# Performance work log

Measured on AMD Instinct MI355X. Metric: run time of the kernel, lower is better.

## Reference

```python
import jax, jax.numpy as jnp
import numpy as np

B, T, N, M = 64, 128, 128, 512


def setup_inputs() -> dict:
    key = jax.random.key(0)
    ks = jax.random.split(key, 9)
    w = 0.02
    return dict(
        X=jax.random.normal(ks[0], (B, T, N), jnp.float32),
        h0=jax.random.normal(ks[1], (B, M), jnp.float32) * 0.05,
        s0=jax.random.normal(ks[2], (B, M), jnp.float32) * 0.05,
        # LSTM cell params (keras gate order: i, f, c, o)
        W_lstm=jax.random.normal(ks[3], (N, 4 * M), jnp.float32) * w,
        U_lstm=jax.random.normal(ks[4], (M, 4 * M), jnp.float32) * w,
        b_lstm=jnp.zeros((4 * M,), jnp.float32),
        # InputAttention params: W_e: Dense(T) on concat([h,c]) (2m -> T),
        # U_e: Dense(T) on X^T (T -> T), v_e: Dense(1) (T -> 1)
        W_e=jax.random.normal(ks[5], (2 * M, T), jnp.float32) * w,
        b_We=jnp.zeros((T,), jnp.float32),
        U_e=jax.random.normal(ks[6], (T, T), jnp.float32) * w,
        b_Ue=jnp.zeros((T,), jnp.float32),
        v_e=jax.random.normal(ks[7], (T, 1), jnp.float32) * w,
        b_ve=jnp.zeros((1,), jnp.float32),
    )


def reference(X, h0, s0, W_lstm, U_lstm, b_lstm, W_e, b_We, U_e, b_Ue, v_e, b_ve):
    # In the original, every loop iteration t runs a single LSTM step on
    # X[:, t, :] starting from the SAME initial_state [h0, s0] (state is not
    # carried across t), so all T steps are independent -> vectorize over T.
    z = jnp.einsum('btn,nk->btk', X, W_lstm) + (h0 @ U_lstm + b_lstm)[:, None, :]
    zi, zf, zc, zo = jnp.split(z, 4, axis=-1)  # keras gate order i,f,c,o
    i = jax.nn.sigmoid(zi)
    f = jax.nn.sigmoid(zf)
    o = jax.nn.sigmoid(zo)
    c = f * s0[:, None, :] + i * jnp.tanh(zc)  # (B, T, m)
    h = o * jnp.tanh(c)                        # (B, T, m)

    # InputAttention for every t at once:
    # e_t = v_e(tanh(W_e([h_t; c_t]) broadcast over n  +  U_e(X^T)))
    hc = jnp.concatenate([h, c], axis=-1)              # (B, T, 2m)
    A = hc @ W_e + b_We                                # (B, T, T)
    U = jnp.einsum('btn,tk->bnk', X, U_e) + b_Ue       # (B, n, T)
    e = jnp.tanh(A[:, :, None, :] + U[:, None, :, :])  # (B, T, n, T)
    scores = jnp.einsum('btnk,k->btn', e, v_e[:, 0]) + b_ve[0]  # (B, T, n)
    alpha = jax.nn.softmax(scores, axis=-1)            # softmax over n
    return X * alpha
```

## Files before the change

kernel.cpp:

```cpp
#include <hip/hip_runtime.h>

typedef __attribute__((ext_vector_type(8))) short bfrag;
typedef __attribute__((ext_vector_type(4))) float f32x4;

#define C_SCALE 2.885390081777926815f

__device__ __forceinline__ float fast_rcp(float x){
#if __has_builtin(__builtin_amdgcn_rcpf)
  return __builtin_amdgcn_rcpf(x);
#else
  return 1.0f/x;
#endif
}
__device__ __forceinline__ float fexp2(float x){
#if __has_builtin(__builtin_amdgcn_exp2f)
  return __builtin_amdgcn_exp2f(x);
#else
  return exp2f(x);
#endif
}
__device__ __forceinline__ float sigm(float x){ return fast_rcp(1.0f + __expf(-x)); }
__device__ __forceinline__ float tanh_f(float x){ return 1.0f - 2.0f*fast_rcp(__expf(2.0f*x) + 1.0f); }
__device__ __forceinline__ unsigned short f2bf(float f){
  unsigned u = __float_as_uint(f);
  return (unsigned short)((u + 0x7fffu + ((u>>16)&1u)) >> 16);
}
__device__ __forceinline__ void gload16(const void* g, void* l){
  __builtin_amdgcn_global_load_lds((const __attribute__((address_space(1))) void*)g,
                                   (__attribute__((address_space(3))) void*)l, 16, 0, 0);
}

__global__ __launch_bounds__(256) void prep(const float* __restrict__ X,
                                            unsigned short* __restrict__ Xbf,
                                            const float* __restrict__ Wl,
                                            unsigned short* __restrict__ Wlt,
                                            const float* __restrict__ We,
                                            unsigned short* __restrict__ Wet,
                                            const float* __restrict__ h0,
                                            const float* __restrict__ Ul,
                                            float* __restrict__ Uhp,
                                            const float* __restrict__ Ue,
                                            const float* __restrict__ bUe,
                                            unsigned short* __restrict__ UTb){
  __shared__ __align__(16) float sh[6600];
  const int tid = threadIdx.x;
  const int bid = blockIdx.x;

  if (bid < 512){
    const int i = (bid*256 + tid)*8;
    float4 a = *(const float4*)&X[i];
    float4 b = *(const float4*)&X[i+4];
    ushort4 lo, hi;
    lo.x=f2bf(a.x); lo.y=f2bf(a.y); lo.z=f2bf(a.z); lo.w=f2bf(a.w);
    hi.x=f2bf(b.x); hi.y=f2bf(b.y); hi.z=f2bf(b.z); hi.w=f2bf(b.w);
    *(ushort4*)&Xbf[i] = lo; *(ushort4*)&Xbf[i+4] = hi;
  } else if (bid < 608){
    const float* in; unsigned short* outp; int K, N, j0, k0, perm;
    if (bid < 576){ int r = bid-512; in = Wl; outp = Wlt; K = 128;  N = 2048; j0 = (r&31)*64; k0 = (r>>5)*64; perm = 0; }
    else          { int r = bid-576; in = We; outp = Wet; K = 1024; N = 128;  j0 = (r&1)*64;  k0 = (r>>1)*64; perm = 1; }
    float (*t)[68] = (float(*)[68])sh;
#pragma unroll
    for (int i=0;i<4;i++){
      int idx = tid + i*256;
      int r = idx>>4, c4 = idx&15;
      int kk = k0 + r;
      int srow = perm ? ((kk&1) ? 512 + (kk>>1) : (kk>>1)) : kk;
      *(float4*)&t[r][c4*4] = *(const float4*)&in[srow*N + j0 + c4*4];
    }
    __syncthreads();
#pragma unroll
    for (int i=0;i<4;i++){
      int idx = tid + i*256;
      int r = idx>>4, c4 = idx&15;
      ushort4 o;
      o.x = f2bf(t[c4*4+0][r]); o.y = f2bf(t[c4*4+1][r]);
      o.z = f2bf(t[c4*4+2][r]); o.w = f2bf(t[c4*4+3][r]);
      *(ushort4*)&outp[(j0+r)*K + k0 + c4*4] = o;
    }
  } else if (bid < 736){
    const int r = bid - 608;
    const int nh = r & 1, b = r >> 1;
    float (*Xs)[68]  = (float(*)[68])sh;
    float (*Us)[132] = (float(*)[132])(sh + 2176);
    const int tc5 = tid & 31, tr8 = tid >> 5;
    f32x4 a4[8];
#pragma unroll
    for (int j=0;j<8;j++) a4[j] = (f32x4){0.f,0.f,0.f,0.f};
    for (int tk=0; tk<4; tk++){
#pragma unroll
      for (int i=0;i<2;i++){
        int idx = tid + i*256;
        int t = idx>>4, nq = idx&15;
        *(float4*)&Xs[t][nq*4] = *(const float4*)&X[(b*128 + tk*32 + t)*128 + nh*64 + nq*4];
      }
#pragma unroll
      for (int i=0;i<4;i++){
        int idx = tid + i*256;
        int t = idx>>5, kq = idx&31;
        *(float4*)&Us[t][kq*4] = *(const float4*)&Ue[(tk*32+t)*128 + kq*4];
      }
      __syncthreads();
#pragma unroll 4
      for (int t=0;t<32;t++){
        f32x4 u4 = *(const f32x4*)&Us[t][tc5*4];
        f32x4 x0 = *(const f32x4*)&Xs[t][tr8*8];
        f32x4 x1 = *(const f32x4*)&Xs[t][tr8*8+4];
        a4[0] += x0.x*u4; a4[1] += x0.y*u4; a4[2] += x0.z*u4; a4[3] += x0.w*u4;
        a4[4] += x1.x*u4; a4[5] += x1.y*u4; a4[6] += x1.z*u4; a4[7] += x1.w*u4;
      }
      __syncthreads();
    }
    const f32x4 bu = *(const f32x4*)&bUe[tc5*4];
    const int ktile = tc5 >> 1, khalf = tc5 & 1;
#pragma unroll
    for (int j=0;j<8;j++){
      const int n = nh*64 + tr8*8 + j;
      f32x4 v = a4[j] + bu;
      ushort4 o;
      o.x = f2bf(fexp2(C_SCALE*v.x)); o.y = f2bf(fexp2(C_SCALE*v.y));
      o.z = f2bf(fexp2(C_SCALE*v.z)); o.w = f2bf(fexp2(C_SCALE*v.w));
      *(ushort4*)&UTb[b*16384 + ktile*1024 + n*8 + khalf*4] = o;
    }
  } else {
    const int r = bid - 736;
    const int jc = r & 15;
    const int bc = (r>>4) >> 2, kc = (r>>4) & 3;
    float (*h0s)[128] = (float(*)[128])sh;
#pragma unroll
    for (int i=0;i<2;i++){
      int idx = tid + i*256;
      int bi = idx>>5, kq = idx&31;
      *(float4*)&h0s[bi][kq*4] = *(const float4*)&h0[(bc*16+bi)*512 + kc*128 + kq*4];
    }
    __syncthreads();
    const int jj = tid & 127, bh = tid >> 7;
    const int j = jc*128 + jj;
    float acc[8];
#pragma unroll
    for (int i=0;i<8;i++) acc[i]=0.f;
    for (int k=0;k<128;k+=4){
      float w0 = Ul[(kc*128+k+0)*2048 + j];
      float w1 = Ul[(kc*128+k+1)*2048 + j];
      float w2 = Ul[(kc*128+k+2)*2048 + j];
      float w3 = Ul[(kc*128+k+3)*2048 + j];
#pragma unroll
      for (int bi=0;bi<8;bi++){
        float4 h4 = *(const float4*)&h0s[bh*8+bi][k];
        acc[bi] += h4.x*w0 + h4.y*w1 + h4.z*w2 + h4.w*w3;
      }
    }
#pragma unroll
    for (int bi=0;bi<8;bi++)
      Uhp[kc*131072 + (bc*16 + bh*8 + bi)*2048 + j] = acc[bi];
  }
}

__global__ __launch_bounds__(256) void k2_k(const unsigned short* __restrict__ Xbf,
                                            const unsigned short* __restrict__ Wlt,
                                            const float* __restrict__ Uhp,
                                            const float* __restrict__ bl,
                                            const float* __restrict__ s0,
                                            unsigned int* __restrict__ hci){
  __shared__ __align__(16) char lds[32768];
  const int tid = threadIdx.x;
  const int mc = blockIdx.x & 15, b = blockIdx.x >> 4;
  const int bt0 = b*128;
  const int lane = tid & 63, wave = tid >> 6;
  const int wr = wave >> 1, wc = wave & 1;

  f32x4 acc[4][4];
#pragma unroll
  for (int mt=0;mt<4;mt++)
#pragma unroll
    for (int nt=0;nt<4;nt++) acc[mt][nt] = (f32x4){0.f,0.f,0.f,0.f};

  for (int kh=0; kh<2; kh++){
#pragma unroll
    for (int i=0;i<4;i++){
      int g = tid + i*256;
      int r = g>>3, G = g&7;
      gload16(Xbf + (bt0+r)*128 + kh*64 + ((G ^ (r&7))<<3), lds + g*16);
    }
#pragma unroll
    for (int i=0;i<4;i++){
      int g = tid + i*256;
      int c = g>>3, G = g&7;
      int q = c>>4;
      int j = (q&3)*512 + mc*32 + ((q>>2)<<4) + (c&15);
      gload16(Wlt + j*128 + kh*64 + ((G ^ (c&7))<<3), lds + 16384 + g*16);
    }
    __syncthreads();
#pragma unroll
    for (int ks2=0; ks2<2; ks2++){
      const int kb = ks2*64 + ((lane>>4)<<4);
      bfrag a[4], bb[4];
#pragma unroll
      for (int mt=0;mt<4;mt++){
        int r = wr*64 + mt*16 + (lane&15);
        a[mt] = *(const bfrag*)&lds[r*128 + (kb ^ ((r&7)<<4))];
      }
#pragma unroll
      for (int nt=0;nt<4;nt++){
        int c = wc*64 + nt*16 + (lane&15);
        bb[nt] = *(const bfrag*)&lds[16384 + c*128 + (kb ^ ((c&7)<<4))];
      }
#pragma unroll
      for (int mt=0;mt<4;mt++)
#pragma unroll
        for (int nt=0;nt<4;nt++)
          acc[mt][nt] = __builtin_amdgcn_mfma_f32_16x16x32_bf16(a[mt], bb[nt], acc[mt][nt], 0, 0, 0);
    }
    __syncthreads();
  }

  const int mloc = mc*32 + wc*16 + (lane&15);
  float uh[4];
#pragma unroll
  for (int g=0;g<4;g++){
    int j = g*512 + mloc;
    uh[g] = bl[j] + Uhp[0*131072 + b*2048 + j] + Uhp[1*131072 + b*2048 + j]
                  + Uhp[2*131072 + b*2048 + j] + Uhp[3*131072 + b*2048 + j];
  }
  const float s0v = s0[b*512 + mloc];
#pragma unroll
  for (int mt=0;mt<4;mt++){
#pragma unroll
    for (int reg=0;reg<4;reg++){
      int row = wr*64 + mt*16 + (lane>>4)*4 + reg;
      float zi = acc[mt][0][reg] + uh[0];
      float zf = acc[mt][1][reg] + uh[1];
      float zc = acc[mt][2][reg] + uh[2];
      float zo = acc[mt][3][reg] + uh[3];
      float fi = sigm(zi), ff = sigm(zf), fo = sigm(zo);
      float cv = ff*s0v + fi*tanh_f(zc);
      float hv = fo*tanh_f(cv);
      hci[(bt0+row)*512 + mloc] = (unsigned)f2bf(hv) | ((unsigned)f2bf(cv) << 16);
    }
  }
}

__global__ __launch_bounds__(256) void k35(const unsigned short* __restrict__ hc,
                                           const unsigned short* __restrict__ Wet,
                                           const float* __restrict__ bWe,
                                           const float* __restrict__ X,
                                           const unsigned short* __restrict__ UTb,
                                           const float* __restrict__ ve,
                                           float* __restrict__ out){
  __shared__ __align__(16) char ldsA[4096];
  __shared__ __align__(16) char ldsB[32768];
  __shared__ __align__(16) float eAs[16][132];
  __shared__ __align__(16) float vs[128];
  __shared__ float redm[4][8], reds[4][8];
  const int tid = threadIdx.x;
  const int tpc = blockIdx.x;
  const int b   = blockIdx.y;
  const int t0  = tpc*16;
  const int lane = tid & 63, wave = tid >> 6;

  if (tid < 128) vs[tid] = ve[tid];

  f32x4 acc[2];
  acc[0] = (f32x4){0.f,0.f,0.f,0.f};
  acc[1] = (f32x4){0.f,0.f,0.f,0.f};

  for (int ks=0; ks<8; ks++){
    const int k0 = ks*128;
    {
      int r = tid>>4, G = tid&15;
      gload16(hc + (b*128 + t0 + r)*1024 + k0 + ((G ^ (r&7))<<3), ldsA + tid*16);
    }
#pragma unroll
    for (int i=0;i<8;i++){
      int g = tid + i*256;
      int n = g>>4, G = g&15;
      gload16(Wet + n*1024 + k0 + ((G ^ (n&7))<<3), ldsB + g*16);
    }
    __syncthreads();
#pragma unroll
    for (int kk=0;kk<4;kk++){
      const int kb = kk*64 + ((lane>>4)<<4);
      const int r = lane & 15;
      bfrag a = *(const bfrag*)&ldsA[r*256 + (kb ^ ((r&7)<<4))];
      const int c0 = wave*32 + (lane&15);
      bfrag b0 = *(const bfrag*)&ldsB[c0*256 + (kb ^ ((c0&7)<<4))];
      const int c1 = c0 + 16;
      bfrag b1 = *(const bfrag*)&ldsB[c1*256 + (kb ^ ((c1&7)<<4))];
      acc[0] = __builtin_amdgcn_mfma_f32_16x16x32_bf16(a, b0, acc[0], 0, 0, 0);
      acc[1] = __builtin_amdgcn_mfma_f32_16x16x32_bf16(a, b1, acc[1], 0, 0, 0);
    }
    __syncthreads();
  }
#pragma unroll
  for (int nt=0;nt<2;nt++){
    const int col = wave*32 + nt*16 + (lane&15);
    const float bw = bWe[col];
#pragma unroll
    for (int reg=0;reg<4;reg++){
      const int row = (lane>>4)*4 + reg;
      eAs[row][col] = fexp2(C_SCALE*(acc[nt][reg] + bw));
    }
  }
  __syncthreads();

  const int tpair = tid>>7, n = tid&127, wid = tid>>6;
  f32x4 sc[8];
#pragma unroll
  for (int tt=0;tt<8;tt++) sc[tt] = (f32x4){0.f,0.f,0.f,0.f};

  const unsigned short* urow = UTb + b*16384 + n*8;
#pragma unroll 2
  for (int k8=0; k8<16; k8++){
    uint4 u = *(const uint4*)(urow + k8*1024);
    f32x4 ua, ub;
    ua.x = __uint_as_float(u.x<<16); ua.y = __uint_as_float(u.x & 0xffff0000u);
    ua.z = __uint_as_float(u.y<<16); ua.w = __uint_as_float(u.y & 0xffff0000u);
    ub.x = __uint_as_float(u.z<<16); ub.y = __uint_as_float(u.z & 0xffff0000u);
    ub.z = __uint_as_float(u.w<<16); ub.w = __uint_as_float(u.w & 0xffff0000u);
    const f32x4 va = *(const f32x4*)&vs[k8*8];
    const f32x4 vb = *(const f32x4*)&vs[k8*8+4];
#pragma unroll
    for (int tt=0; tt<8; tt++){
      const float* Ar = &eAs[tt*2+tpair][k8*8];
      f32x4 ea = *(const f32x4*)Ar;
      f32x4 eb = *(const f32x4*)(Ar+4);
      f32x4 ra, rb;
      ra.x = fast_rcp(ea.x*ua.x + 1.f); ra.y = fast_rcp(ea.y*ua.y + 1.f);
      ra.z = fast_rcp(ea.z*ua.z + 1.f); ra.w = fast_rcp(ea.w*ua.w + 1.f);
      rb.x = fast_rcp(eb.x*ub.x + 1.f); rb.y = fast_rcp(eb.y*ub.y + 1.f);
      rb.z = fast_rcp(eb.z*ub.z + 1.f); rb.w = fast_rcp(eb.w*ub.w + 1.f);
      sc[tt] += va*ra;
      sc[tt] += vb*rb;
    }
  }

  float sv[8];
#pragma unroll
  for (int tt=0;tt<8;tt++){
    float s = -2.f*((sc[tt].x + sc[tt].y) + (sc[tt].z + sc[tt].w));
    sv[tt] = s;
    float m = s;
#pragma unroll
    for (int off=32; off>0; off>>=1) m = fmaxf(m, __shfl_xor(m, off));
    if ((tid&63)==0) redm[wid][tt] = m;
  }
  __syncthreads();
  float evv[8];
#pragma unroll
  for (int tt=0;tt<8;tt++){
    const float M = fmaxf(redm[tpair*2][tt], redm[tpair*2+1][tt]);
    float e = __expf(sv[tt] - M);
    evv[tt] = e;
    float s = e;
#pragma unroll
    for (int off=32; off>0; off>>=1) s += __shfl_xor(s, off);
    if ((tid&63)==0) reds[wid][tt] = s;
  }
  __syncthreads();
#pragma unroll
  for (int tt=0;tt<8;tt++){
    const float S = reds[tpair*2][tt] + reds[tpair*2+1][tt];
    const float alpha = evv[tt] * fast_rcp(S);
    const int t = t0 + tt*2 + tpair;
    const int g = (b*128 + t)*128 + n;
    out[g] = X[g] * alpha;
  }
}

extern "C" void kernel_launch(void* const* d_in, const int* in_sizes, int n_in,
                              void* d_out, int out_size, void* d_ws, size_t ws_size,
                              hipStream_t stream){
  (void)in_sizes; (void)n_in; (void)out_size; (void)ws_size;
  const float* X   = (const float*)d_in[0];
  const float* h0  = (const float*)d_in[1];
  const float* s0  = (const float*)d_in[2];
  const float* Wl  = (const float*)d_in[3];
  const float* Ul  = (const float*)d_in[4];
  const float* bl  = (const float*)d_in[5];
  const float* We  = (const float*)d_in[6];
  const float* bWe = (const float*)d_in[7];
  const float* Ue  = (const float*)d_in[8];
  const float* bUe = (const float*)d_in[9];
  const float* ve  = (const float*)d_in[10];
  float* out = (float*)d_out;

  char* ws = (char*)d_ws;
  unsigned short* Wlt = (unsigned short*)(ws + 0);
  unsigned short* Wet = (unsigned short*)(ws + 524288);
  unsigned short* Xbf = (unsigned short*)(ws + 786432);
  unsigned short* UTb = (unsigned short*)(ws + 2883584);
  unsigned short* hc  = (unsigned short*)(ws + 4980736);
  float*          Uhp = (float*)(ws + 21757952);
  unsigned int*   hci = (unsigned int*)hc;

  prep <<<dim3(992),   256, 0, stream>>>(X, Xbf, Wl, Wlt, We, Wet, h0, Ul, Uhp, Ue, bUe, UTb);
  k2_k <<<dim3(1024),  256, 0, stream>>>(Xbf, Wlt, Uhp, bl, s0, hci);
  k35  <<<dim3(8,64),  256, 0, stream>>>(hc, Wet, bWe, X, UTb, ve, out);
}
```

Measured before the change: 65.04 us.

## Process 32 time rows per block in attention kernel to reuse W_e tile

Doubles the number of time rows each k35 block handles, from 16 to 32, and halves the grid. The W_e^T tile streamed through LDS is then reused across twice as many rows. The GEMM uses a 2x2 wave layout with four accumulators per wave, and the score/softmax stage runs two halves of 8 rows each. LDS buffers are unioned so the exp(A) table aliases the GEMM staging area. The trade-off is fewer blocks for the GPU's compute units and more registers per thread.

```diff
diff --git a/kernel.cpp b/kernel.cpp
--- a/kernel.cpp
+++ b/kernel.cpp
@@ -246,122 +246,131 @@
                                            const unsigned short* __restrict__ UTb,
                                            const float* __restrict__ ve,
                                            float* __restrict__ out){
-  __shared__ __align__(16) char ldsA[4096];
-  __shared__ __align__(16) char ldsB[32768];
-  __shared__ __align__(16) float eAs[16][132];
+  __shared__ __align__(16) char lds[40960];
   __shared__ __align__(16) float vs[128];
-  __shared__ float redm[4][8], reds[4][8];
+  __shared__ float redm[4][16], reds[4][16];
   const int tid = threadIdx.x;
   const int tpc = blockIdx.x;
   const int b   = blockIdx.y;
-  const int t0  = tpc*16;
+  const int bt0 = b*128 + tpc*32;
   const int lane = tid & 63, wave = tid >> 6;
+  const int wr = wave >> 1, wc = wave & 1;
 
   if (tid < 128) vs[tid] = ve[tid];
 
-  f32x4 acc[2];
-  acc[0] = (f32x4){0.f,0.f,0.f,0.f};
-  acc[1] = (f32x4){0.f,0.f,0.f,0.f};
+  f32x4 acc[4];
+#pragma unroll
+  for (int nt=0;nt<4;nt++) acc[nt] = (f32x4){0.f,0.f,0.f,0.f};
+
+  char* ldsA = lds;
+  char* ldsB = lds + 8192;
 
   for (int ks=0; ks<8; ks++){
     const int k0 = ks*128;
-    {
-      int r = tid>>4, G = tid&15;
-      gload16(hc + (b*128 + t0 + r)*1024 + k0 + ((G ^ (r&7))<<3), ldsA + tid*16);
+#pragma unroll
+    for (int i=0;i<2;i++){
+      int g = tid + i*256;
+      int r = g>>4, G = g&15;
+      gload16(hc + (bt0+r)*1024 + k0 + ((G ^ (r&7))<<3), ldsA + g*16);
     }
 #pragma unroll
     for (int i=0;i<8;i++){
       int g = tid + i*256;
-      int n = g>>4, G = g&15;
-      gload16(Wet + n*1024 + k0 + ((G ^ (n&7))<<3), ldsB + g*16);
+      int nn = g>>4, G = g&15;
+      gload16(Wet + nn*1024 + k0 + ((G ^ (nn&7))<<3), ldsB + g*16);
     }
     __syncthreads();
 #pragma unroll
     for (int kk=0;kk<4;kk++){
       const int kb = kk*64 + ((lane>>4)<<4);
-      const int r = lane & 15;
+      const int r = wr*16 + (lane&15);
       bfrag a = *(const bfrag*)&ldsA[r*256 + (kb ^ ((r&7)<<4))];
-      const int c0 = wave*32 + (lane&15);
-      bfrag b0 = *(const bfrag*)&ldsB[c0*256 + (kb ^ ((c0&7)<<4))];
-      const int c1 = c0 + 16;
-      bfrag b1 = *(const bfrag*)&ldsB[c1*256 + (kb ^ ((c1&7)<<4))];
-      acc[0] = __builtin_amdgcn_mfma_f32_16x16x32_bf16(a, b0, acc[0], 0, 0, 0);
-      acc[1] = __builtin_amdgcn_mfma_f32_16x16x32_bf16(a, b1, acc[1], 0, 0, 0);
-    }
-    __syncthreads();
-  }
-#pragma unroll
-  for (int nt=0;nt<2;nt++){
-    const int col = wave*32 + nt*16 + (lane&15);
+#pragma unroll
+      for (int nt=0;nt<4;nt++){
+        const int c = wc*64 + nt*16 + (lane&15);
+        bfrag bv = *(const bfrag*)&ldsB[c*256 + (kb ^ ((c&7)<<4))];
+        acc[nt] = __builtin_amdgcn_mfma_f32_16x16x32_bf16(a, bv, acc[nt], 0, 0, 0);
+      }
+    }
+    __syncthreads();
+  }
+
+  float (*eAs)[132] = (float(*)[132])lds;
+#pragma unroll
+  for (int nt=0;nt<4;nt++){
+    const int col = wc*64 + nt*16 + (lane&15);
     const float bw = bWe[col];
 #pragma unroll
     for (int reg=0;reg<4;reg++){
-      const int row = (lane>>4)*4 + reg;
+      const int row = wr*16 + (lane>>4)*4 + reg;
       eAs[row][col] = fexp2(C_SCALE*(acc[nt][reg] + bw));
     }
   }
   __syncthreads();
 
   const int tpair = tid>>7, n = tid&127, wid = tid>>6;
-  f32x4 sc[8];
-#pragma unroll
-  for (int tt=0;tt<8;tt++) sc[tt] = (f32x4){0.f,0.f,0.f,0.f};
-
   const unsigned short* urow = UTb + b*16384 + n*8;
+  float sv[16];
+
+#pragma unroll
+  for (int half=0; half<2; half++){
+    f32x4 sc[8];
+#pragma unroll
+    for (int tt=0;tt<8;tt++) sc[tt] = (f32x4){0.f,0.f,0.f,0.f};
 #pragma unroll 2
-  for (int k8=0; k8<16; k8++){
-    uint4 u = *(const uint4*)(urow + k8*1024);
-    f32x4 ua, ub;
-    ua.x = __uint_as_float(u.x<<16); ua.y = __uint_as_float(u.x & 0xffff0000u);
-    ua.z = __uint_as_float(u.y<<16); ua.w = __uint_as_float(u.y & 0xffff0000u);
-    ub.x = __uint_as_float(u.z<<16); ub.y = __uint_as_float(u.z & 0xffff0000u);
-    ub.z = __uint_as_float(u.w<<16); ub.w = __uint_as_float(u.w & 0xffff0000u);
-    const f32x4 va = *(const f32x4*)&vs[k8*8];
-    const f32x4 vb = *(const f32x4*)&vs[k8*8+4];
-#pragma unroll
-    for (int tt=0; tt<8; tt++){
-      const float* Ar = &eAs[tt*2+tpair][k8*8];
-      f32x4 ea = *(const f32x4*)Ar;
-      f32x4 eb = *(const f32x4*)(Ar+4);
-      f32x4 ra, rb;
-      ra.x = fast_rcp(ea.x*ua.x + 1.f); ra.y = fast_rcp(ea.y*ua.y + 1.f);
-      ra.z = fast_rcp(ea.z*ua.z + 1.f); ra.w = fast_rcp(ea.w*ua.w + 1.f);
-      rb.x = fast_rcp(eb.x*ub.x + 1.f); rb.y = fast_rcp(eb.y*ub.y + 1.f);
-      rb.z = fast_rcp(eb.z*ub.z + 1.f); rb.w = fast_rcp(eb.w*ub.w + 1.f);
-      sc[tt] += va*ra;
-      sc[tt] += vb*rb;
-    }
-  }
-
-  float sv[8];
-#pragma unroll
-  for (int tt=0;tt<8;tt++){
-    float s = -2.f*((sc[tt].x + sc[tt].y) + (sc[tt].z + sc[tt].w));
-    sv[tt] = s;
-    float m = s;
+    for (int k8=0; k8<16; k8++){
+      uint4 u = *(const uint4*)(urow + k8*1024);
+      f32x4 ua, ub;
+      ua.x = __uint_as_float(u.x<<16); ua.y = __uint_as_float(u.x & 0xffff0000u);
+      ua.z = __uint_as_float(u.y<<16); ua.w = __uint_as_float(u.y & 0xffff0000u);
+      ub.x = __uint_as_float(u.z<<16); ub.y = __uint_as_float(u.z & 0xffff0000u);
+      ub.z = __uint_as_float(u.w<<16); ub.w = __uint_as_float(u.w & 0xffff0000u);
+      const f32x4 va = *(const f32x4*)&vs[k8*8];
+      const f32x4 vb = *(const f32x4*)&vs[k8*8+4];
+#pragma unroll
+      for (int tt=0; tt<8; tt++){
+        const float* Ar = &eAs[(half*8+tt)*2+tpair][k8*8];
+        f32x4 ea = *(const f32x4*)Ar;
+        f32x4 eb = *(const f32x4*)(Ar+4);
+        f32x4 ra, rb;
+        ra.x = fast_rcp(ea.x*ua.x + 1.f); ra.y = fast_rcp(ea.y*ua.y + 1.f);
+        ra.z = fast_rcp(ea.z*ua.z + 1.f); ra.w = fast_rcp(ea.w*ua.w + 1.f);
+        rb.x = fast_rcp(eb.x*ub.x + 1.f); rb.y = fast_rcp(eb.y*ub.y + 1.f);
+        rb.z = fast_rcp(eb.z*ub.z + 1.f); rb.w = fast_rcp(eb.w*ub.w + 1.f);
+        sc[tt] += va*ra;
+        sc[tt] += vb*rb;
+      }
+    }
+#pragma unroll
+    for (int tt=0;tt<8;tt++)
+      sv[half*8+tt] = -2.f*((sc[tt].x + sc[tt].y) + (sc[tt].z + sc[tt].w));
+  }
+
+#pragma unroll
+  for (int st=0;st<16;st++){
+    float m = sv[st];
 #pragma unroll
     for (int off=32; off>0; off>>=1) m = fmaxf(m, __shfl_xor(m, off));
-    if ((tid&63)==0) redm[wid][tt] = m;
+    if ((tid&63)==0) redm[wid][st] = m;
   }
   __syncthreads();
-  float evv[8];
-#pragma unroll
-  for (int tt=0;tt<8;tt++){
-    const float M = fmaxf(redm[tpair*2][tt], redm[tpair*2+1][tt]);
-    float e = __expf(sv[tt] - M);
-    evv[tt] = e;
+  float evv[16];
+#pragma unroll
+  for (int st=0;st<16;st++){
+    const float M = fmaxf(redm[tpair*2][st], redm[tpair*2+1][st]);
+    float e = __expf(sv[st] - M);
+    evv[st] = e;
     float s = e;
 #pragma unroll
     for (int off=32; off>0; off>>=1) s += __shfl_xor(s, off);
-    if ((tid&63)==0) reds[wid][tt] = s;
+    if ((tid&63)==0) reds[wid][st] = s;
   }
   __syncthreads();
 #pragma unroll
-  for (int tt=0;tt<8;tt++){
-    const float S = reds[tpair*2][tt] + reds[tpair*2+1][tt];
-    const float alpha = evv[tt] * fast_rcp(S);
-    const int t = t0 + tt*2 + tpair;
-    const int g = (b*128 + t)*128 + n;
+  for (int st=0;st<16;st++){
+    const float S = reds[tpair*2][st] + reds[tpair*2+1][st];
+    const float alpha = evv[st] * fast_rcp(S);
+    const int g = (bt0 + st*2 + tpair)*128 + n;
     out[g] = X[g] * alpha;
   }
 }
@@ -394,5 +403,5 @@
 
   prep <<<dim3(992),   256, 0, stream>>>(X, Xbf, Wl, Wlt, We, Wet, h0, Ul, Uhp, Ue, bUe, UTb);
   k2_k <<<dim3(1024),  256, 0, stream>>>(Xbf, Wlt, Uhp, bl, s0, hci);
-  k35  <<<dim3(8,64),  256, 0, stream>>>(hc, Wet, bWe, X, UTb, ve, out);
-}
+  k35  <<<dim3(4,64),  256, 0, stream>>>(hc, Wet, bWe, X, UTb, ve, out);
+}
```

Measured after the change: 79.30 us. +21.9%, slower.
